# Optimization experiments

Hardware: AMD Instinct MI355X
Metric: run time of the kernel (lower is better)

The kernel has to match this reference:

```python
import jax, jax.numpy as jnp
import numpy as np

N = 100000
E = 1600000
D_IN, D_HID, D_OUT = 128, 256, 128


def setup_inputs() -> dict:
    key = jax.random.key(0)
    ks = jax.random.split(key, 8)
    x = jax.random.normal(ks[0], (N, D_IN), dtype=jnp.float32)
    edge_index = jax.random.randint(ks[1], (2, E), 0, N, dtype=jnp.int64)
    # PyG SAGEConv params: lin_l (applied to aggregated neighbors, has bias),
    # lin_r (applied to root/self, no bias). Stored as [in, out] for x @ W.
    s0 = 1.0 / np.sqrt(D_IN)
    s1 = 1.0 / np.sqrt(D_HID)
    Wl0 = jax.random.uniform(ks[2], (D_IN, D_HID), jnp.float32, -s0, s0)
    bl0 = jnp.zeros((D_HID,), jnp.float32)
    Wr0 = jax.random.uniform(ks[3], (D_IN, D_HID), jnp.float32, -s0, s0)
    Wl1 = jax.random.uniform(ks[4], (D_HID, D_OUT), jnp.float32, -s1, s1)
    bl1 = jnp.zeros((D_OUT,), jnp.float32)
    Wr1 = jax.random.uniform(ks[5], (D_HID, D_OUT), jnp.float32, -s1, s1)
    return {"x": x, "edge_index": edge_index, "Wl0": Wl0, "bl0": bl0,
            "Wr0": Wr0, "Wl1": Wl1, "bl1": bl1, "Wr1": Wr1}


def _sage_conv(x, src, dst, W_l, b_l, W_r, num_nodes):
    # mean-aggregate source features at destination nodes
    msg = x[src]                                         # [E, d] gather
    agg = jax.ops.segment_sum(msg, dst, num_segments=num_nodes)  # [N, d]
    deg = jax.ops.segment_sum(jnp.ones((src.shape[0],), x.dtype), dst,
                              num_segments=num_nodes)    # [N]
    agg = agg / jnp.maximum(deg, 1.0)[:, None]
    return agg @ W_l + b_l + x @ W_r                     # [N, out]


def reference(x, edge_index, Wl0, bl0, Wr0, Wl1, bl1, Wr1):
    src, dst = edge_index[0], edge_index[1]
    n = x.shape[0]
    h = _sage_conv(x, src, dst, Wl0, bl0, Wr0, n)
    h = jax.nn.relu(h)  # dropout is identity in eval mode
    out = _sage_conv(h, src, dst, Wl1, bl1, Wr1, n)
    return out
```

## Files before the change

### kernel.cpp

```cpp
#include <hip/hip_runtime.h>

typedef short bf16x8 __attribute__((ext_vector_type(8)));
typedef float f32x4 __attribute__((ext_vector_type(4)));
typedef unsigned int uint;
typedef unsigned short ushort;
typedef ushort u16x8 __attribute__((ext_vector_type(8)));
typedef uint u32x2 __attribute__((ext_vector_type(2)));
typedef uint u32x4 __attribute__((ext_vector_type(4)));

#define NBLK 256
#define LCAP 24576
#define HP 264

__device__ inline ushort f2bf(float f) {
    uint u = __builtin_bit_cast(uint, f);
    uint r = u + 0x7fffu + ((u >> 16) & 1u);
    return (ushort)(r >> 16);
}
__device__ inline float bf2f(uint lo16) {
    uint u = lo16 << 16;
    return __builtin_bit_cast(float, u);
}
__device__ inline float bf2f_hi(uint v) {
    uint u = v & 0xffff0000u;
    return __builtin_bit_cast(float, u);
}

__device__ inline void packw_body(const float* __restrict__ Wa, const float* __restrict__ Wb,
                                  ushort* __restrict__ out, int mode, int tile, int l) {
    int cb = tile >> 3, ks = tile & 7;
    int col = cb * 16 + (l & 15);
    int k0 = ks * 32 + ((l >> 4) * 8);
    ushort vals[8];
#pragma unroll
    for (int j = 0; j < 8; j++) {
        int k = k0 + j;
        float f;
        if (mode == 0)
            f = (k < 128) ? Wa[(size_t)k * 256 + col] : Wb[(size_t)(k - 128) * 256 + col];
        else
            f = (col < 128) ? Wa[(size_t)k * 128 + col] : Wb[(size_t)k * 128 + (col - 128)];
        vals[j] = f2bf(f);
    }
    ushort* dst = out + ((size_t)(ks * 16 + cb) * 64 + l) * 8;
#pragma unroll
    for (int j = 0; j < 8; j++) dst[j] = vals[j];
}

__global__ void prep_kernel(const float* __restrict__ x, ushort* __restrict__ a1,
                            const float* __restrict__ Wr0, const float* __restrict__ Wl0,
                            ushort* __restrict__ w1p,
                            const float* __restrict__ Wl1, const float* __restrict__ Wr1,
                            ushort* __restrict__ w2p,
                            const int* __restrict__ dst, int* __restrict__ ghist,
                            int E, int CE, int NB, int n) {
    __shared__ int hist[512];
    int bb = blockIdx.x;
    int tid = threadIdx.x;
    if (bb < NBLK) {
        for (int b = tid; b < NB; b += 256) hist[b] = 0;
        __syncthreads();
        int start = bb * CE, end = min(E, start + CE);
        for (int e = start + tid; e < end; e += 256) {
            int d = dst[e];
            atomicAdd(&hist[d >> 8], 1);
        }
        __syncthreads();
        for (int b = tid; b < NB; b += 256) ghist[(size_t)b * NBLK + bb] = hist[b];
    } else if (bb < NBLK + 64) {
        int r = bb - NBLK;
        int tile = (r & 31) * 4 + (tid >> 6);
        int l = tid & 63;
        if (r < 32) packw_body(Wr0, Wl0, w1p, 0, tile, l);
        else        packw_body(Wl1, Wr1, w2p, 1, tile, l);
    } else {
        int i = (bb - NBLK - 64) * 256 + tid;
        int total = n * 32;
        if (i < total) {
            int row = i >> 5, q = i & 31;
            float4 v = *(const float4*)(x + (size_t)row * 128 + q * 4);
            ushort4 o;
            o.x = f2bf(v.x); o.y = f2bf(v.y); o.z = f2bf(v.z); o.w = f2bf(v.w);
            *(ushort4*)(a1 + (size_t)row * 256 + q * 4) = o;
        }
    }
}

__global__ void scan1_kernel(const int* __restrict__ cnt, int* __restrict__ rs,
                             int* __restrict__ bsum, int n) {
    __shared__ int tmp[256];
    int tid = threadIdx.x;
    int idx = blockIdx.x * 256 + tid;
    int v = (idx < n) ? cnt[idx] : 0;
    tmp[tid] = v;
    __syncthreads();
#pragma unroll
    for (int off = 1; off < 256; off <<= 1) {
        int t = (tid >= off) ? tmp[tid - off] : 0;
        __syncthreads();
        tmp[tid] += t;
        __syncthreads();
    }
    if (idx < n) rs[idx] = tmp[tid] - v;
    if (tid == 255) bsum[blockIdx.x] = tmp[255];
}

__global__ void scan23_kernel(int* __restrict__ rs, const int* __restrict__ bsum,
                              int n, int E) {
    __shared__ int red[256];
    int tid = threadIdx.x;
    int b = blockIdx.x;
    int s = 0;
    for (int t = tid; t < b; t += 256) s += bsum[t];
    red[tid] = s;
    __syncthreads();
#pragma unroll
    for (int off = 128; off > 0; off >>= 1) {
        if (tid < off) red[tid] += red[tid + off];
        __syncthreads();
    }
    int offv = red[0];
    int idx = b * 256 + tid;
    if (idx < n) rs[idx] += offv;
    if (b == 0 && tid == 0) rs[n] = E;
}

__global__ void p3_kernel(const int* __restrict__ src, const int* __restrict__ dst,
                          const int* __restrict__ goff, uint* __restrict__ ebuck,
                          int E, int CE, int NB) {
    __shared__ int cur[512];
    int tid = threadIdx.x;
    for (int b = tid; b < NB; b += 256) cur[b] = goff[(size_t)b * NBLK + blockIdx.x];
    __syncthreads();
    int start = blockIdx.x * CE, end = min(E, start + CE);
    for (int e = start + tid; e < end; e += 256) {
        int d = dst[e];
        int s = src[e];
        int slot = atomicAdd(&cur[d >> 8], 1);
        ebuck[slot] = ((uint)(d & 255) << 17) | (uint)s;
    }
}

__global__ void p4_kernel(const uint* __restrict__ ebuck, const int* __restrict__ goff,
                          int* __restrict__ rs, int* __restrict__ nbr, int n, int E, int NB) {
    __shared__ uint ebuf[LCAP];
    __shared__ int cnt[256];
    __shared__ int cur[256];
    int tid = threadIdx.x;
    int b = blockIdx.x;
    int d0 = b << 8;
    int eb = goff[(size_t)b * NBLK];
    int ee = (b == NB - 1) ? E : goff[(size_t)(b + 1) * NBLK];
    cnt[tid] = 0;
    __syncthreads();
    int m = ee - eb;
    for (int i = tid; i < m; i += 256) {
        uint v = ebuck[eb + i];
        if (i < LCAP) ebuf[i] = v;
        atomicAdd(&cnt[v >> 17], 1);
    }
    __syncthreads();
    int v0 = cnt[tid];
    cur[tid] = v0;
    __syncthreads();
#pragma unroll
    for (int off = 1; off < 256; off <<= 1) {
        int t = (tid >= off) ? cur[tid - off] : 0;
        __syncthreads();
        cur[tid] += t;
        __syncthreads();
    }
    int excl = cur[tid] - v0;
    int node = d0 + tid;
    if (node < n) rs[node] = eb + excl;
    if (b == NB - 1 && tid == 0) rs[n] = E;
    __syncthreads();
    cur[tid] = eb + excl;
    __syncthreads();
    for (int i = tid; i < m; i += 256) {
        uint v = (i < LCAP) ? ebuf[i] : ebuck[eb + i];
        int p = atomicAdd(&cur[v >> 17], 1);
        nbr[p] = (int)(v & 0x1FFFFu);
    }
}

__launch_bounds__(512, 1)
__global__ void fused_gemm_kernel(const ushort* __restrict__ A, const ushort* __restrict__ W1,
                                  const ushort* __restrict__ W2, const float* __restrict__ b0,
                                  const float* __restrict__ b1, ushort* __restrict__ zb,
                                  float* __restrict__ outf, int n) {
    extern __shared__ unsigned char smem[];
    unsigned char* regW = smem;
    ushort* H = (ushort*)(smem + 65536);
    int tid = threadIdx.x;
    int l = tid & 63, w = tid >> 6;
    int q = l >> 4;
    int row0 = blockIdx.x * 128;
    int lrow16 = l & 15;
    int grow = row0 + w * 16 + lrow16;
    if (grow > n - 1) grow = n - 1;
    ushort* hpriv = H + (size_t)w * (16 * HP);

    const unsigned char* wsrc0 = (const unsigned char*)W1;
    const unsigned char* wsrc1 = (const unsigned char*)W1 + 65536;
    const unsigned char* wsrc2 = (const unsigned char*)W2;
    const unsigned char* wsrc3 = (const unsigned char*)W2 + 65536;

    bf16x8 a[8];
    {
        const ushort* ap = A + (size_t)grow * 256 + q * 8;
#pragma unroll
        for (int ks = 0; ks < 8; ks++) a[ks] = *(const bf16x8*)(ap + ks * 32);
    }
    u32x4 wr[8];
#pragma unroll
    for (int i = 0; i < 8; i++) wr[i] = *(const u32x4*)(wsrc0 + (size_t)i * 8192 + tid * 16);
#pragma unroll
    for (int i = 0; i < 8; i++) *(u32x4*)(regW + i * 8192 + tid * 16) = wr[i];

    f32x4 acc[16];
#pragma unroll
    for (int cb = 0; cb < 16; cb++) acc[cb] = (f32x4){0.f, 0.f, 0.f, 0.f};

    __syncthreads();

#pragma unroll
    for (int c = 0; c < 4; c++) {
        if (c == 0) {
#pragma unroll
            for (int i = 0; i < 8; i++) wr[i] = *(const u32x4*)(wsrc1 + (size_t)i * 8192 + tid * 16);
        } else if (c == 1) {
#pragma unroll
            for (int i = 0; i < 8; i++) wr[i] = *(const u32x4*)(wsrc2 + (size_t)i * 8192 + tid * 16);
        } else if (c == 2) {
#pragma unroll
            for (int i = 0; i < 8; i++) wr[i] = *(const u32x4*)(wsrc3 + (size_t)i * 8192 + tid * 16);
        }
        int hb = c & 1;
#pragma unroll
        for (int cb = 0; cb < 16; cb++) {
#pragma unroll
            for (int ksl = 0; ksl < 4; ksl++) {
                bf16x8 b = *(const bf16x8*)(regW + ((size_t)(ksl * 16 + cb) * 64 + l) * 16);
                acc[cb] = __builtin_amdgcn_mfma_f32_16x16x32_bf16(b, a[hb * 4 + ksl], acc[cb], 0, 0, 0);
            }
        }
        if (c == 1) {
#pragma unroll
            for (int cb = 0; cb < 16; cb++) {
                int colb = cb * 16 + q * 4;
                f32x4 bv = *(const f32x4*)(b0 + colb);
                f32x4 v = acc[cb];
                float v0 = fmaxf(v[0] + bv[0], 0.f);
                float v1 = fmaxf(v[1] + bv[1], 0.f);
                float v2 = fmaxf(v[2] + bv[2], 0.f);
                float v3 = fmaxf(v[3] + bv[3], 0.f);
                u32x2 pk;
                pk[0] = (uint)f2bf(v0) | ((uint)f2bf(v1) << 16);
                pk[1] = (uint)f2bf(v2) | ((uint)f2bf(v3) << 16);
                *(u32x2*)(hpriv + (size_t)lrow16 * HP + colb) = pk;
            }
#pragma unroll
            for (int ks = 0; ks < 8; ks++)
                a[ks] = *(const bf16x8*)(hpriv + (size_t)lrow16 * HP + ks * 32 + q * 8);
#pragma unroll
            for (int cb = 0; cb < 16; cb++) acc[cb] = (f32x4){0.f, 0.f, 0.f, 0.f};
        }
        __syncthreads();
        if (c < 3) {
#pragma unroll
            for (int i = 0; i < 8; i++) *(u32x4*)(regW + i * 8192 + tid * 16) = wr[i];
        }
        __syncthreads();
    }

    int rbase = row0 + w * 16;
#pragma unroll
    for (int cb = 0; cb < 8; cb++) {
        int colb = cb * 16 + q * 4;
        f32x4 v = acc[cb];
        u32x2 pk;
        pk[0] = (uint)f2bf(v[0]) | ((uint)f2bf(v[1]) << 16);
        pk[1] = (uint)f2bf(v[2]) | ((uint)f2bf(v[3]) << 16);
        *(u32x2*)&hpriv[lrow16 * 136 + colb] = pk;
    }
    {
        int rr = l >> 2, qq = l & 3;
        int row = rbase + rr;
#pragma unroll
        for (int rep = 0; rep < 4; rep++) {
            u16x8 vv = *(const u16x8*)&hpriv[rr * 136 + qq * 8 + rep * 32];
            if (row < n)
                *(u16x8*)(zb + (size_t)row * 128 + qq * 8 + rep * 32) = vv;
        }
    }
    int orow = rbase + lrow16;
#pragma unroll
    for (int cb = 8; cb < 16; cb++) {
        int colb = (cb - 8) * 16 + q * 4;
        f32x4 bv = *(const f32x4*)(b1 + colb);
        f32x4 v = acc[cb];
        v[0] += bv[0]; v[1] += bv[1]; v[2] += bv[2]; v[3] += bv[3];
        if (orow < n)
            *(f32x4*)(outf + (size_t)orow * 128 + colb) = v;
    }
}

template <int ADD>
__global__ void segmean_kernel(const uint* __restrict__ fp, int half,
                               const int* __restrict__ rs, const int* __restrict__ nbr,
                               uint* __restrict__ outb, float* __restrict__ outf, int n) {
    int w = threadIdx.x >> 6;
    int l = threadIdx.x & 63;
    int i = blockIdx.x * 4 + w;
    if (i >= n) return;
    int b = rs[i], e = rs[i + 1];
    int q = l & 31;
    int hsel = l >> 5;
    int stride2 = half >> 1;
    const uint2* fpq = (const uint2*)fp + q;
    float a0 = 0.f, a1 = 0.f, a2 = 0.f, a3 = 0.f;
    int j = b;
    for (; j + 8 <= e; j += 8) {
        int s[4];
#pragma unroll
        for (int p = 0; p < 4; p++) s[p] = nbr[j + 2 * p + hsel];
        uint2 v[4];
#pragma unroll
        for (int p = 0; p < 4; p++) v[p] = fpq[(size_t)s[p] * stride2];
#pragma unroll
        for (int p = 0; p < 4; p++) {
            a0 += bf2f(v[p].x & 0xffffu); a1 += bf2f_hi(v[p].x);
            a2 += bf2f(v[p].y & 0xffffu); a3 += bf2f_hi(v[p].y);
        }
    }
    for (; j + 2 <= e; j += 2) {
        int s = nbr[j + hsel];
        uint2 v = fpq[(size_t)s * stride2];
        a0 += bf2f(v.x & 0xffffu); a1 += bf2f_hi(v.x);
        a2 += bf2f(v.y & 0xffffu); a3 += bf2f_hi(v.y);
    }
    if (j < e && hsel == 0) {
        int s = nbr[j];
        uint2 v = fpq[(size_t)s * stride2];
        a0 += bf2f(v.x & 0xffffu); a1 += bf2f_hi(v.x);
        a2 += bf2f(v.y & 0xffffu); a3 += bf2f_hi(v.y);
    }
    a0 += __shfl_xor(a0, 32);
    a1 += __shfl_xor(a1, 32);
    a2 += __shfl_xor(a2, 32);
    a3 += __shfl_xor(a3, 32);
    if (hsel == 0) {
        int dg = e - b;
        float inv = 1.0f / (float)(dg > 1 ? dg : 1);
        a0 *= inv; a1 *= inv; a2 *= inv; a3 *= inv;
        if (ADD) {
            float* op = outf + (size_t)i * (2 * half) + q * 4;
            f32x4 o = *(const f32x4*)op;
            o[0] += a0; o[1] += a1; o[2] += a2; o[3] += a3;
            *(f32x4*)op = o;
        } else {
            u32x2 pk;
            pk[0] = (uint)f2bf(a0) | ((uint)f2bf(a1) << 16);
            pk[1] = (uint)f2bf(a2) | ((uint)f2bf(a3) << 16);
            *(u32x2*)(outb + (size_t)i * half + q * 2) = pk;
        }
    }
}


extern "C" void kernel_launch(void* const* d_in, const int* in_sizes, int n_in,
                              void* d_out, int out_size, void* d_ws, size_t ws_size,
                              hipStream_t stream) {
    const float* x = (const float*)d_in[0];
    const int* ei = (const int*)d_in[1];
    const float* Wl0 = (const float*)d_in[2];
    const float* bl0 = (const float*)d_in[3];
    const float* Wr0 = (const float*)d_in[4];
    const float* Wl1 = (const float*)d_in[5];
    const float* bl1 = (const float*)d_in[6];
    const float* Wr1 = (const float*)d_in[7];
    float* outp = (float*)d_out;

    int n = in_sizes[0] / 128;
    int E = in_sizes[1] / 2;
    const int* srcv = ei;
    const int* dstv = ei + E;

    int NB = (n + 255) >> 8;
    int NG = NB * NBLK;
    int CE = (E + NBLK - 1) / NBLK;

    char* w = (char*)d_ws;
    auto align = [](size_t v) { return (v + 255) & ~(size_t)255; };
    size_t off = 0;
    int* rs    = (int*)(w + off); off = align(off + (size_t)(n + 1) * 4);
    int* bsum2 = (int*)(w + off); off = align(off + (size_t)512 * 4);
    int* ghist = (int*)(w + off); off = align(off + (size_t)(NG + 1) * 4);
    int* goff  = (int*)(w + off); off = align(off + (size_t)(NG + 1) * 4);
    uint* ebuck = (uint*)(w + off); off = align(off + (size_t)E * 4);
    int* nbr   = (int*)(w + off); off = align(off + (size_t)E * 4);
    ushort* a1  = (ushort*)(w + off); off = align(off + (size_t)n * 256 * 2);
    ushort* zb  = (ushort*)(w + off); off = align(off + (size_t)n * 128 * 2);
    ushort* w1p = (ushort*)(w + off); off = align(off + (size_t)256 * 256 * 2);
    ushort* w2p = (ushort*)(w + off); off = align(off + (size_t)256 * 256 * 2);
    (void)ws_size; (void)n_in; (void)out_size;

    int nb2 = (NG + 255) / 256;
    int ncx = (n * 32 + 255) / 256;

    prep_kernel<<<NBLK + 64 + ncx, 256, 0, stream>>>(x, a1, Wr0, Wl0, w1p, Wl1, Wr1, w2p,
                                                     dstv, ghist, E, CE, NB, n);
    scan1_kernel<<<nb2, 256, 0, stream>>>(ghist, goff, bsum2, NG);
    scan23_kernel<<<nb2, 256, 0, stream>>>(goff, bsum2, NG, E);
    p3_kernel<<<NBLK, 256, 0, stream>>>(srcv, dstv, goff, ebuck, E, CE, NB);
    p4_kernel<<<NB, 256, 0, stream>>>(ebuck, goff, rs, nbr, n, E, NB);

    int segb = (n + 3) / 4;
    int mb = (n + 127) / 128;
    int ldsz = 65536 + 8 * 16 * HP * 2;

    hipFuncSetAttribute((const void*)fused_gemm_kernel,
                        hipFuncAttributeMaxDynamicSharedMemorySize, ldsz);

    segmean_kernel<0><<<segb, 256, 0, stream>>>((const uint*)a1, 128, rs, nbr,
                                                (uint*)(a1 + 128), nullptr, n);
    fused_gemm_kernel<<<mb, 512, ldsz, stream>>>(a1, w1p, w2p, bl0, bl1, zb, outp, n);
    segmean_kernel<1><<<segb, 256, 0, stream>>>((const uint*)zb, 64, rs, nbr,
                                                nullptr, outp, n);
}
```

Measured before the change: 256.5 us.

## Keep weight fragments in registers and stage activation rows in LDS

The fused two-layer GEMM kernel is reorganized so that each wave owns two 16-column output blocks and holds the matching weight fragments in registers. Previously the weights were streamed through LDS in four chunks, and each wave kept its own 16 rows of activations in registers. Now the block's 128 activation rows are loaded into LDS once, and every wave reads all rows from there. This removes the repeated weight copies to LDS, cuts barriers, and shrinks LDS use to about 66KB. In exchange it adds LDS reads of activations by all waves and raises register pressure.

```diff
diff --git a/kernel.cpp b/kernel.cpp
--- a/kernel.cpp
+++ b/kernel.cpp
@@ -189,120 +189,132 @@
                                   const ushort* __restrict__ W2, const float* __restrict__ b0,
                                   const float* __restrict__ b1, ushort* __restrict__ zb,
                                   float* __restrict__ outf, int n) {
-    extern __shared__ unsigned char smem[];
-    unsigned char* regW = smem;
-    ushort* H = (ushort*)(smem + 65536);
+    extern __shared__ ushort H[];
     int tid = threadIdx.x;
     int l = tid & 63, w = tid >> 6;
-    int q = l >> 4;
+    int q = l >> 4, r16 = l & 15;
     int row0 = blockIdx.x * 128;
-    int lrow16 = l & 15;
-    int grow = row0 + w * 16 + lrow16;
-    if (grow > n - 1) grow = n - 1;
-    ushort* hpriv = H + (size_t)w * (16 * HP);
-
-    const unsigned char* wsrc0 = (const unsigned char*)W1;
-    const unsigned char* wsrc1 = (const unsigned char*)W1 + 65536;
-    const unsigned char* wsrc2 = (const unsigned char*)W2;
-    const unsigned char* wsrc3 = (const unsigned char*)W2 + 65536;
-
-    bf16x8 a[8];
+
     {
-        const ushort* ap = A + (size_t)grow * 256 + q * 8;
-#pragma unroll
-        for (int ks = 0; ks < 8; ks++) a[ks] = *(const bf16x8*)(ap + ks * 32);
-    }
-    u32x4 wr[8];
-#pragma unroll
-    for (int i = 0; i < 8; i++) wr[i] = *(const u32x4*)(wsrc0 + (size_t)i * 8192 + tid * 16);
-#pragma unroll
-    for (int i = 0; i < 8; i++) *(u32x4*)(regW + i * 8192 + tid * 16) = wr[i];
-
-    f32x4 acc[16];
-#pragma unroll
-    for (int cb = 0; cb < 16; cb++) acc[cb] = (f32x4){0.f, 0.f, 0.f, 0.f};
-
-    __syncthreads();
-
-#pragma unroll
-    for (int c = 0; c < 4; c++) {
-        if (c == 0) {
-#pragma unroll
-            for (int i = 0; i < 8; i++) wr[i] = *(const u32x4*)(wsrc1 + (size_t)i * 8192 + tid * 16);
-        } else if (c == 1) {
-#pragma unroll
-            for (int i = 0; i < 8; i++) wr[i] = *(const u32x4*)(wsrc2 + (size_t)i * 8192 + tid * 16);
-        } else if (c == 2) {
-#pragma unroll
-            for (int i = 0; i < 8; i++) wr[i] = *(const u32x4*)(wsrc3 + (size_t)i * 8192 + tid * 16);
-        }
-        int hb = c & 1;
-#pragma unroll
-        for (int cb = 0; cb < 16; cb++) {
-#pragma unroll
-            for (int ksl = 0; ksl < 4; ksl++) {
-                bf16x8 b = *(const bf16x8*)(regW + ((size_t)(ksl * 16 + cb) * 64 + l) * 16);
-                acc[cb] = __builtin_amdgcn_mfma_f32_16x16x32_bf16(b, a[hb * 4 + ksl], acc[cb], 0, 0, 0);
+        int rr = tid >> 5;
+        int cc = (tid & 31) * 8;
+#pragma unroll
+        for (int it = 0; it < 8; it++) {
+            int lr = it * 16 + rr;
+            int row = row0 + lr;
+            if (row > n - 1) row = n - 1;
+            u32x4 v = *(const u32x4*)(A + (size_t)row * 256 + cc);
+            *(u32x4*)(&H[(size_t)lr * HP + cc]) = v;
+        }
+    }
+
+    bf16x8 bf1[2][8];
+#pragma unroll
+    for (int cbi = 0; cbi < 2; cbi++) {
+        int cb = 2 * w + cbi;
+#pragma unroll
+        for (int ks = 0; ks < 8; ks++)
+            bf1[cbi][ks] = *(const bf16x8*)(W1 + ((size_t)((ks * 16 + cb) * 64 + l)) * 8);
+    }
+
+    f32x4 acc[8][2];
+#pragma unroll
+    for (int rg = 0; rg < 8; rg++)
+#pragma unroll
+        for (int cbi = 0; cbi < 2; cbi++) acc[rg][cbi] = (f32x4){0.f, 0.f, 0.f, 0.f};
+
+    __syncthreads();
+
+#pragma unroll
+    for (int rg = 0; rg < 8; rg++) {
+        bf16x8 a[8];
+        const ushort* hp = &H[(size_t)(rg * 16 + r16) * HP + q * 8];
+#pragma unroll
+        for (int ks = 0; ks < 8; ks++) a[ks] = *(const bf16x8*)(hp + ks * 32);
+#pragma unroll
+        for (int cbi = 0; cbi < 2; cbi++)
+#pragma unroll
+            for (int ks = 0; ks < 8; ks++)
+                acc[rg][cbi] = __builtin_amdgcn_mfma_f32_16x16x32_bf16(bf1[cbi][ks], a[ks],
+                                                                       acc[rg][cbi], 0, 0, 0);
+    }
+
+    bf16x8 bf2[2][8];
+#pragma unroll
+    for (int cbi = 0; cbi < 2; cbi++) {
+        int cb = 2 * w + cbi;
+#pragma unroll
+        for (int ks = 0; ks < 8; ks++)
+            bf2[cbi][ks] = *(const bf16x8*)(W2 + ((size_t)((ks * 16 + cb) * 64 + l)) * 8);
+    }
+
+    __syncthreads();
+
+#pragma unroll
+    for (int rg = 0; rg < 8; rg++) {
+#pragma unroll
+        for (int cbi = 0; cbi < 2; cbi++) {
+            int colb = (2 * w + cbi) * 16 + q * 4;
+            f32x4 bv = *(const f32x4*)(b0 + colb);
+            f32x4 v = acc[rg][cbi];
+            float v0 = fmaxf(v[0] + bv[0], 0.f);
+            float v1 = fmaxf(v[1] + bv[1], 0.f);
+            float v2 = fmaxf(v[2] + bv[2], 0.f);
+            float v3 = fmaxf(v[3] + bv[3], 0.f);
+            u32x2 pk;
+            pk[0] = (uint)f2bf(v0) | ((uint)f2bf(v1) << 16);
+            pk[1] = (uint)f2bf(v2) | ((uint)f2bf(v3) << 16);
+            *(u32x2*)(&H[(size_t)(rg * 16 + r16) * HP + colb]) = pk;
+            acc[rg][cbi] = (f32x4){0.f, 0.f, 0.f, 0.f};
+        }
+    }
+
+    __syncthreads();
+
+#pragma unroll
+    for (int rg = 0; rg < 8; rg++) {
+        bf16x8 a[8];
+        const ushort* hp = &H[(size_t)(rg * 16 + r16) * HP + q * 8];
+#pragma unroll
+        for (int ks = 0; ks < 8; ks++) a[ks] = *(const bf16x8*)(hp + ks * 32);
+#pragma unroll
+        for (int cbi = 0; cbi < 2; cbi++)
+#pragma unroll
+            for (int ks = 0; ks < 8; ks++)
+                acc[rg][cbi] = __builtin_amdgcn_mfma_f32_16x16x32_bf16(bf2[cbi][ks], a[ks],
+                                                                       acc[rg][cbi], 0, 0, 0);
+    }
+
+    if (w < 4) {
+#pragma unroll
+        for (int rg = 0; rg < 8; rg++) {
+            int row = row0 + rg * 16 + r16;
+#pragma unroll
+            for (int cbi = 0; cbi < 2; cbi++) {
+                int colb = (2 * w + cbi) * 16 + q * 4;
+                f32x4 v = acc[rg][cbi];
+                u32x2 pk;
+                pk[0] = (uint)f2bf(v[0]) | ((uint)f2bf(v[1]) << 16);
+                pk[1] = (uint)f2bf(v[2]) | ((uint)f2bf(v[3]) << 16);
+                if (row < n)
+                    *(u32x2*)(zb + (size_t)row * 128 + colb) = pk;
             }
         }
-        if (c == 1) {
-#pragma unroll
-            for (int cb = 0; cb < 16; cb++) {
-                int colb = cb * 16 + q * 4;
-                f32x4 bv = *(const f32x4*)(b0 + colb);
-                f32x4 v = acc[cb];
-                float v0 = fmaxf(v[0] + bv[0], 0.f);
-                float v1 = fmaxf(v[1] + bv[1], 0.f);
-                float v2 = fmaxf(v[2] + bv[2], 0.f);
-                float v3 = fmaxf(v[3] + bv[3], 0.f);
-                u32x2 pk;
-                pk[0] = (uint)f2bf(v0) | ((uint)f2bf(v1) << 16);
-                pk[1] = (uint)f2bf(v2) | ((uint)f2bf(v3) << 16);
-                *(u32x2*)(hpriv + (size_t)lrow16 * HP + colb) = pk;
+    } else {
+        int wq = w - 4;
+#pragma unroll
+        for (int rg = 0; rg < 8; rg++) {
+            int row = row0 + rg * 16 + r16;
+#pragma unroll
+            for (int cbi = 0; cbi < 2; cbi++) {
+                int colb = 32 * wq + cbi * 16 + q * 4;
+                f32x4 bv = *(const f32x4*)(b1 + colb);
+                f32x4 v = acc[rg][cbi];
+                v[0] += bv[0]; v[1] += bv[1]; v[2] += bv[2]; v[3] += bv[3];
+                if (row < n)
+                    *(f32x4*)(outf + (size_t)row * 128 + colb) = v;
             }
-#pragma unroll
-            for (int ks = 0; ks < 8; ks++)
-                a[ks] = *(const bf16x8*)(hpriv + (size_t)lrow16 * HP + ks * 32 + q * 8);
-#pragma unroll
-            for (int cb = 0; cb < 16; cb++) acc[cb] = (f32x4){0.f, 0.f, 0.f, 0.f};
-        }
-        __syncthreads();
-        if (c < 3) {
-#pragma unroll
-            for (int i = 0; i < 8; i++) *(u32x4*)(regW + i * 8192 + tid * 16) = wr[i];
-        }
-        __syncthreads();
-    }
-
-    int rbase = row0 + w * 16;
-#pragma unroll
-    for (int cb = 0; cb < 8; cb++) {
-        int colb = cb * 16 + q * 4;
-        f32x4 v = acc[cb];
-        u32x2 pk;
-        pk[0] = (uint)f2bf(v[0]) | ((uint)f2bf(v[1]) << 16);
-        pk[1] = (uint)f2bf(v[2]) | ((uint)f2bf(v[3]) << 16);
-        *(u32x2*)&hpriv[lrow16 * 136 + colb] = pk;
-    }
-    {
-        int rr = l >> 2, qq = l & 3;
-        int row = rbase + rr;
-#pragma unroll
-        for (int rep = 0; rep < 4; rep++) {
-            u16x8 vv = *(const u16x8*)&hpriv[rr * 136 + qq * 8 + rep * 32];
-            if (row < n)
-                *(u16x8*)(zb + (size_t)row * 128 + qq * 8 + rep * 32) = vv;
-        }
-    }
-    int orow = rbase + lrow16;
-#pragma unroll
-    for (int cb = 8; cb < 16; cb++) {
-        int colb = (cb - 8) * 16 + q * 4;
-        f32x4 bv = *(const f32x4*)(b1 + colb);
-        f32x4 v = acc[cb];
-        v[0] += bv[0]; v[1] += bv[1]; v[2] += bv[2]; v[3] += bv[3];
-        if (orow < n)
-            *(f32x4*)(outf + (size_t)orow * 128 + colb) = v;
+        }
     }
 }
 
@@ -418,7 +430,7 @@
 
     int segb = (n + 3) / 4;
     int mb = (n + 127) / 128;
-    int ldsz = 65536 + 8 * 16 * HP * 2;
+    int ldsz = 128 * HP * 2;
 
     hipFuncSetAttribute((const void*)fused_gemm_kernel,
                         hipFuncAttributeMaxDynamicSharedMemorySize, ldsz);
```

Result: faster. 248.6 us (-3.1%).
